# Kernel optimization log

Measured on AMD Instinct MI355X. Metric: run time of the kernel, lower is better.

## Reference

```python
import jax, jax.numpy as jnp
import numpy as np

B, T1, S, M = 64, 129, 128, 32   # batch, time-major dim, seq_len, num_series
U = 256                           # SkipGRUUnits
SKIP = 4                          # skip
HW = 128                          # highway window (== S by shape constraints)


def _skip_lstm(x_seq, kernel, rkernel, kernel2, bias, bias2, s0, units, skip):
    """Run the bespoke skip-LSTM cell over time. x_seq: (B, T, D) -> (B, T, U)."""
    Bx = x_seq.shape[0]
    # precompute input projections for all timesteps: (B, T, 4U)
    xW = jnp.einsum('btd,du->btu', x_seq, kernel) + bias
    # recurrent kernel viewed per-gate: Rk[:, g, :] == rkernel[:, g*U:(g+1)*U]
    Rk = rkernel.reshape(units, 4, units)

    def step(carry, x_t):
        h_tm1, c_tm1, prev_h = carry            # (B,4U), (B,U), (B,U*skip)
        x_i, x_f, x_c, x_o = jnp.split(x_t, 4, axis=1)
        hg = h_tm1.reshape(Bx, 4, units)        # gate-specific previous state
        r = jnp.einsum('bgu,ugv->bgv', hg, Rk)  # (B,4,U)
        i = jax.nn.sigmoid(x_i + r[:, 0])
        f = jax.nn.sigmoid(x_f + r[:, 1])
        c = f * c_tm1 + i * jnp.tanh(x_c + r[:, 2])
        o = jax.nn.sigmoid(x_o + r[:, 3])
        h = o * jnp.tanh(c)
        h_skip = jax.nn.sigmoid(prev_h[:, :units] @ kernel2 + bias2)
        h = s0 * h + (1.0 - s0) * h_skip
        new_h_tm1 = jnp.concatenate([i, f, c, o], axis=1)
        new_prev = jnp.concatenate([prev_h[:, units:], h], axis=1)
        return (new_h_tm1, c, new_prev), h

    init = (jnp.zeros((Bx, 4 * units), x_seq.dtype),
            jnp.zeros((Bx, units), x_seq.dtype),
            jnp.zeros((Bx, units * skip), x_seq.dtype))
    _, hs = jax.lax.scan(step, init, jnp.swapaxes(xW, 0, 1))  # (T,B,U)
    return jnp.swapaxes(hs, 0, 1)


def setup_inputs() -> dict:
    key = jax.random.key(0)
    ks = jax.random.split(key, 10)
    g = lambda k, shape, s=0.05: (jax.random.normal(k, shape, jnp.float32) * s)
    return {
        'X': jax.random.normal(ks[0], (B, T1, S, M), jnp.float32),
        'enc_kernel': g(ks[1], (M, 4 * U)),
        'enc_rkernel': g(ks[2], (U, 4 * U)),
        'enc_kernel2': g(ks[3], (U, U)),
        'enc_bias': jnp.zeros((4 * U,), jnp.float32),
        'enc_bias2': jnp.zeros((U,), jnp.float32),
        'enc_s0': jnp.float32(0.5),
        'dec_kernel': g(ks[4], (U, 4 * U)),
        'dec_rkernel': g(ks[5], (U, 4 * U)),
        'dec_kernel2': g(ks[6], (U, U)),
        'dec_bias': jnp.zeros((4 * U,), jnp.float32),
        'dec_bias2': jnp.zeros((U,), jnp.float32),
        'dec_s0': jnp.float32(0.5),
        'dense_w': g(ks[7], (S * U, S * M), 0.01),
        'dense_b': jnp.zeros((S * M,), jnp.float32),
        'final_w': g(ks[8], (HW,), 0.05),
        'final_b': jnp.zeros((), jnp.float32),
    }


def reference(X, enc_kernel, enc_rkernel, enc_kernel2, enc_bias, enc_bias2, enc_s0,
              dec_kernel, dec_rkernel, dec_kernel2, dec_bias, dec_bias2, dec_s0,
              dense_w, dense_b, final_w, final_b):
    X1 = X[:, 0]        # (B, S, M) encoder input
    X2 = X[:, 1:]       # (B, T1-1, S, M) highway inputs
    SE = _skip_lstm(X1, enc_kernel, enc_rkernel, enc_kernel2, enc_bias, enc_bias2, enc_s0, U, SKIP)
    SD = _skip_lstm(SE, dec_kernel, dec_rkernel, dec_kernel2, dec_bias, dec_bias2, dec_s0, U, SKIP)
    RD = SD.reshape(X.shape[0], S * U)
    Y = (RD @ dense_w + dense_b).reshape(-1, S, M)  # (B, S, M)
    # highway: PreARTrans takes last HW steps, shared final Linear(S->1) over time axis
    Z2 = jnp.einsum('bism,s->bim', X2[:, :, -HW:, :], final_w) + final_b  # (B, T1-1, M)
    return Y + Z2
```

## Files before the change

### kernel.cpp

```cpp
#include <hip/hip_runtime.h>
#include <hip/hip_fp16.h>


__device__ __forceinline__ float sigmoidf_(float x) {
    return 1.0f / (1.0f + __expf(-x));
}
__device__ __forceinline__ float tanhf_(float x) {
    float xc = fminf(fmaxf(x, -15.f), 15.f);
    float e = __expf(2.f * xc);
    return (e - 1.f) / (e + 1.f);
}
__device__ __forceinline__ unsigned pkh(float lo, float hi) {
    __half2 h = __halves2half2(__float2half(lo), __float2half(hi));
    return *reinterpret_cast<unsigned*>(&h);
}
__device__ __forceinline__ float2 uph(unsigned u) {
    __half2 h = *reinterpret_cast<__half2*>(&u);
    return __half22float2(h);
}

__global__ __launch_bounds__(256) void packall(
    const float* __restrict__ e_rk, const float* __restrict__ d_rk,
    const float* __restrict__ d_k,  const float* __restrict__ e_k,
    const float* __restrict__ e_k2, const float* __restrict__ d_k2,
    float4* __restrict__ rk4e, float4* __restrict__ rk4d,
    float4* __restrict__ dk4,  float4* __restrict__ ek4,
    unsigned* __restrict__ kh2e, unsigned* __restrict__ kh2d,
    unsigned* __restrict__ flags)
{
    const int bx = blockIdx.x, v = threadIdx.x;
    if (bx < 800) {
        const float* src; float4* dst; int row;
        if (bx < 256)      { src = e_rk; dst = rk4e; row = bx; }
        else if (bx < 512) { src = d_rk; dst = rk4d; row = bx - 256; }
        else if (bx < 768) { src = d_k;  dst = dk4;  row = bx - 512; }
        else               { src = e_k;  dst = ek4;  row = bx - 768; }
        const float* s = src + (size_t)row * 1024;
        dst[row * 256 + v] = make_float4(s[v], s[256 + v], s[512 + v], s[768 + v]);
    } else if (bx < 928) {
        const int u2 = bx - 800;
        kh2e[u2 * 256 + v] = pkh(e_k2[(2 * u2) * 256 + v], e_k2[(2 * u2 + 1) * 256 + v]);
        kh2d[u2 * 256 + v] = pkh(d_k2[(2 * u2) * 256 + v], d_k2[(2 * u2 + 1) * 256 + v]);
    } else {
        flags[v] = 0u;
    }
}

__global__ __launch_bounds__(256) void xw_gemm_enc(
    const float*  __restrict__ X,
    const float4* __restrict__ ek4,
    const float*  __restrict__ bias,
    float4* __restrict__ xWp)
{
    const int v = threadIdx.x;
    const int r0 = blockIdx.x * 16;
    __shared__ float se[16][32];

    #pragma unroll
    for (int p = 0; p < 2; ++p) {
        int idx = p * 256 + v;
        int rr = idx >> 5, d = idx & 31;
        int R = r0 + rr, b = R >> 7, t = R & 127;
        se[rr][d] = X[((size_t)b * 129 * 128 + t) * 32 + d];
    }
    __syncthreads();

    float4 bv = make_float4(bias[v], bias[256 + v], bias[512 + v], bias[768 + v]);
    float4 acc[16];
    #pragma unroll
    for (int rr = 0; rr < 16; ++rr) acc[rr] = bv;

    #pragma unroll
    for (int u = 0; u < 32; ++u) {
        float4 w = ek4[u * 256 + v];
        #pragma unroll
        for (int rr = 0; rr < 16; ++rr) {
            float s = se[rr][u];
            acc[rr].x += s * w.x; acc[rr].y += s * w.y;
            acc[rr].z += s * w.z; acc[rr].w += s * w.w;
        }
    }
    #pragma unroll
    for (int rr = 0; rr < 16; ++rr)
        xWp[(size_t)(r0 + rr) * 256 + v] = acc[rr];
}

__global__ __launch_bounds__(512) void xw_gemm_dec(
    const float*  __restrict__ SE,
    const float4* __restrict__ dk4,
    const float*  __restrict__ bias,
    float4* __restrict__ xWp)
{
    const int tid = threadIdx.x;
    const int v = tid & 255;
    const int hh = tid >> 8;
    const int rbase = blockIdx.x * 32;
    __shared__ float se[32][256];

    for (int i = tid; i < 8192; i += 512) {
        int rr = i >> 8, c = i & 255;
        se[rr][c] = SE[(size_t)(rbase + rr) * 256 + c];
    }
    __syncthreads();

    float4 bv = make_float4(bias[v], bias[256 + v], bias[512 + v], bias[768 + v]);
    float4 acc[16];
    #pragma unroll
    for (int rr = 0; rr < 16; ++rr) acc[rr] = bv;

    #pragma unroll 8
    for (int u = 0; u < 256; ++u) {
        float4 w = dk4[u * 256 + v];
        #pragma unroll
        for (int rr = 0; rr < 16; ++rr) {
            float s = se[hh * 16 + rr][u];
            acc[rr].x += s * w.x; acc[rr].y += s * w.y;
            acc[rr].z += s * w.z; acc[rr].w += s * w.w;
        }
    }
    #pragma unroll
    for (int rr = 0; rr < 16; ++rr)
        xWp[(size_t)(rbase + hh * 16 + rr) * 256 + v] = acc[rr];
}

__global__ __launch_bounds__(1024, 4) void rec9(
    const float4*   __restrict__ xW,
    const float4*   __restrict__ rk4,
    const unsigned* __restrict__ kh2,
    const float*    __restrict__ bias2,
    const float*    __restrict__ s0p,
    float* __restrict__ out,
    float* __restrict__ EX,
    unsigned* __restrict__ flags,
    unsigned fbase)
{
    const int b     = blockIdx.x & 63;
    const int slice = blockIdx.x >> 6;
    const int voff  = slice * 64;
    const int tid   = threadIdx.x;
    const int us    = tid >> 6;
    const int vl    = tid & 63;
    const int v     = voff + vl;

    __shared__ float4 wres[128][64];
    __shared__ float4 pA[16][64];
    __shared__ float  pS[16][64];
    __shared__ float4 h4[256];
    __shared__ float  pq[4][256];

    for (int i = tid; i < 8192; i += 1024) {
        int r = i >> 6, vv = i & 63;
        int cc = r >> 3, j = r & 7;
        wres[r][vv] = rk4[(cc * 16 + j) * 256 + voff + vv];
    }
    float4 wreg[8];
    unsigned kreg[8];
    {
        const float4*   wp = rk4 + (us * 16 + 8) * 256 + v;
        const unsigned* kp = kh2 + (us * 8) * 256 + v;
        #pragma unroll
        for (int j = 0; j < 8; ++j) wreg[j] = wp[j * 256];
        #pragma unroll
        for (int j = 0; j < 8; ++j) kreg[j] = kp[j * 256];
    }
    if (tid < 256) {
        h4[tid] = make_float4(0.f, 0.f, 0.f, 0.f);
        pq[0][tid] = 0.f; pq[1][tid] = 0.f; pq[2][tid] = 0.f; pq[3][tid] = 0.f;
    }
    float cst = 0.f;
    const float s0 = s0p[0];
    const float b2 = bias2[voff + vl];
    unsigned* mflag = flags + b * 4 + slice;
    __syncthreads();

    for (int t = 0; t < 128; ++t) {
        float4 xa = make_float4(0.f, 0.f, 0.f, 0.f);
        if (tid < 64) xa = xW[((size_t)b * 128 + t) * 256 + voff + tid];
        if (t > 0 && tid < 3) {
            int ps = tid + (tid >= slice ? 1 : 0);
            const unsigned* pf = flags + b * 4 + ps;
            while (__hip_atomic_load(pf, __ATOMIC_RELAXED, __HIP_MEMORY_SCOPE_AGENT) < fbase + (unsigned)t)
                __builtin_amdgcn_s_sleep(2);
        }
        __syncthreads();
        if (t > 0) {
            const int sp = (t + 1) & 1;
            if (tid < 480) {
                int pi = tid / 160;
                int j  = tid - pi * 160;
                int ps = pi + (pi >= slice ? 1 : 0);
                const unsigned long long* src = (const unsigned long long*)
                    (EX + (((size_t)sp * 64 + b) * 4 + ps) * 320);
                unsigned long long d = __hip_atomic_load(src + j, __ATOMIC_RELAXED, __HIP_MEMORY_SCOPE_AGENT);
                if (j < 128) {
                    reinterpret_cast<unsigned long long*>(&h4[ps * 64])[j] = d;
                } else {
                    int k = j - 128;
                    union { unsigned long long u; float f[2]; } cv; cv.u = d;
                    pq[(t + 3) & 3][ps * 64 + 2 * k]     = cv.f[0];
                    pq[(t + 3) & 3][ps * 64 + 2 * k + 1] = cv.f[1];
                }
            }
        }
        __syncthreads();

        float ai = 0.f, af = 0.f, acg = 0.f, ao = 0.f, as = 0.f;
        const int slot = t & 3;
        #pragma unroll
        for (int j = 0; j < 8; ++j) {
            float4 w = wres[us * 8 + j][vl];
            float4 g = h4[us * 16 + j];
            ai += g.x * w.x; af += g.y * w.y; acg += g.z * w.z; ao += g.w * w.w;
        }
        #pragma unroll
        for (int j = 0; j < 8; ++j) {
            float4 w = wreg[j];
            float4 g = h4[us * 16 + 8 + j];
            ai += g.x * w.x; af += g.y * w.y; acg += g.z * w.z; ao += g.w * w.w;
        }
        #pragma unroll
        for (int j = 0; j < 8; ++j) {
            float2 kk = uph(kreg[j]);
            as += pq[slot][us * 16 + 2 * j] * kk.x + pq[slot][us * 16 + 2 * j + 1] * kk.y;
        }
        pA[us][vl] = make_float4(ai, af, acg, ao);
        pS[us][vl] = as;
        __syncthreads();

        if (tid < 64) {
            float4 A = pA[0][vl];
            float  S = pS[0][vl];
            #pragma unroll
            for (int cc = 1; cc < 16; ++cc) {
                float4 q = pA[cc][vl];
                A.x += q.x; A.y += q.y; A.z += q.z; A.w += q.w;
                S += pS[cc][vl];
            }
            float gi = sigmoidf_(xa.x + A.x);
            float gf = sigmoidf_(xa.y + A.y);
            float cb = tanhf_(xa.z + A.z);
            cst = gf * cst + gi * cb;
            float go = sigmoidf_(xa.w + A.w);
            float hh = go * tanhf_(cst);
            float hs = sigmoidf_(S + b2);
            float hf = s0 * hh + (1.f - s0) * hs;
            h4[voff + vl] = make_float4(gi, gf, cst, go);
            pq[slot][voff + vl] = hf;
            out[((size_t)b * 128 + t) * 256 + voff + vl] = hf;
            float* dst = EX + (((size_t)(t & 1) * 64 + b) * 4 + slice) * 320;
            union { float4 f4; unsigned long long u[2]; } gv;
            gv.f4 = make_float4(gi, gf, cst, go);
            __hip_atomic_store((unsigned long long*)dst + 2 * vl,     gv.u[0], __ATOMIC_RELAXED, __HIP_MEMORY_SCOPE_AGENT);
            __hip_atomic_store((unsigned long long*)dst + 2 * vl + 1, gv.u[1], __ATOMIC_RELAXED, __HIP_MEMORY_SCOPE_AGENT);
            __hip_atomic_store(dst + 256 + vl, hf, __ATOMIC_RELAXED, __HIP_MEMORY_SCOPE_AGENT);
        }
        __syncthreads();
        if (tid == 0)
            __hip_atomic_store(mflag, fbase + (unsigned)(t + 1), __ATOMIC_RELAXED, __HIP_MEMORY_SCOPE_AGENT);
    }
}

__global__ __launch_bounds__(512, 4) void dense3(
    const float* __restrict__ SD,
    const float* __restrict__ dw,
    float* __restrict__ P)
{
    const int bid = blockIdx.x;
    const int kc = bid >> 5;
    const int bb = (bid >> 3) & 3;
    const int ct = bid & 7;
    const int tid = threadIdx.x;
    const int wv  = tid >> 6;
    const int wvj = wv & 1;
    const int wv2 = wv >> 1;
    const int lane = tid & 63;
    const int j0 = ct * 512 + wvj * 256 + lane * 4;
    const int kbase = kc * 2048;

    __shared__ float sst[16][68];
    __shared__ float red[4][4][520];

    float4 acc[16];
    #pragma unroll
    for (int b = 0; b < 16; ++b) acc[b] = make_float4(0.f, 0.f, 0.f, 0.f);

    for (int k0 = 0; k0 < 2048; k0 += 64) {
        if (tid < 256) {
            int r = tid >> 4, c4 = (tid & 15) * 4;
            float4 s4 = *reinterpret_cast<const float4*>(
                SD + (size_t)(bb * 16 + r) * 32768 + kbase + k0 + c4);
            sst[r][c4] = s4.x; sst[r][c4 + 1] = s4.y; sst[r][c4 + 2] = s4.z; sst[r][c4 + 3] = s4.w;
        }
        __syncthreads();
        #pragma unroll 2
        for (int kk = 0; kk < 16; ++kk) {
            const int krel = kk * 4 + wv2;
            float4 w4 = *reinterpret_cast<const float4*>(
                dw + (size_t)(kbase + k0 + krel) * 4096 + j0);
            #pragma unroll
            for (int b = 0; b < 16; ++b) {
                float s = sst[b][krel];
                acc[b].x += s * w4.x; acc[b].y += s * w4.y;
                acc[b].z += s * w4.z; acc[b].w += s * w4.w;
            }
        }
        __syncthreads();
    }

    for (int bg = 0; bg < 4; ++bg) {
        __syncthreads();
        #pragma unroll
        for (int i = 0; i < 4; ++i) {
            float4 a = acc[bg * 4 + i];
            float* d = &red[wv2][i][wvj * 256 + lane * 4];
            d[0] = a.x; d[1] = a.y; d[2] = a.z; d[3] = a.w;
        }
        __syncthreads();
        {
            int bi = tid >> 7;
            int jj = (tid & 127) * 4;
            float4 s;
            s.x = red[0][bi][jj]     + red[1][bi][jj]     + red[2][bi][jj]     + red[3][bi][jj];
            s.y = red[0][bi][jj + 1] + red[1][bi][jj + 1] + red[2][bi][jj + 1] + red[3][bi][jj + 1];
            s.z = red[0][bi][jj + 2] + red[1][bi][jj + 2] + red[2][bi][jj + 2] + red[3][bi][jj + 2];
            s.w = red[0][bi][jj + 3] + red[1][bi][jj + 3] + red[2][bi][jj + 3] + red[3][bi][jj + 3];
            *reinterpret_cast<float4*>(
                P + ((size_t)(kc * 64 + bb * 16 + bg * 4 + bi) * 4096) + ct * 512 + jj) = s;
        }
    }
}

__global__ __launch_bounds__(256) void reduce_z2(
    const float* __restrict__ P,
    const float* __restrict__ db,
    const float* __restrict__ X,
    const float* __restrict__ fw,
    const float* __restrict__ fbp,
    float* __restrict__ out)
{
    const int o4 = blockIdx.x * 256 + threadIdx.x;
    const int b  = o4 >> 10;
    const int j4 = o4 & 1023;
    const int j0 = j4 * 4;
    const int i  = j0 >> 5;
    const int m  = j0 & 31;

    float4 acc = *reinterpret_cast<const float4*>(db + j0);
    #pragma unroll
    for (int kc = 0; kc < 16; ++kc) {
        float4 p = *reinterpret_cast<const float4*>(P + (size_t)(kc * 64 + b) * 4096 + j0);
        acc.x += p.x; acc.y += p.y; acc.z += p.z; acc.w += p.w;
    }

    const float* xp = X + ((size_t)(b * 129 + 1 + i) * 128) * 32 + m;
    #pragma unroll 8
    for (int s = 0; s < 128; ++s) {
        float4 xv = *reinterpret_cast<const float4*>(xp + (size_t)s * 32);
        float w = fw[s];
        acc.x += w * xv.x; acc.y += w * xv.y; acc.z += w * xv.z; acc.w += w * xv.w;
    }
    const float fb = fbp[0];
    acc.x += fb; acc.y += fb; acc.z += fb; acc.w += fb;
    *reinterpret_cast<float4*>(out + (size_t)o4 * 4) = acc;
}

extern "C" void kernel_launch(void* const* d_in, const int* in_sizes, int n_in,
                              void* d_out, int out_size, void* d_ws, size_t ws_size,
                              hipStream_t stream) {
    const float* X    = (const float*)d_in[0];
    const float* e_k  = (const float*)d_in[1];
    const float* e_rk = (const float*)d_in[2];
    const float* e_k2 = (const float*)d_in[3];
    const float* e_b  = (const float*)d_in[4];
    const float* e_b2 = (const float*)d_in[5];
    const float* e_s0 = (const float*)d_in[6];
    const float* d_k  = (const float*)d_in[7];
    const float* d_rk = (const float*)d_in[8];
    const float* d_k2 = (const float*)d_in[9];
    const float* d_b  = (const float*)d_in[10];
    const float* d_b2 = (const float*)d_in[11];
    const float* d_s0 = (const float*)d_in[12];
    const float* dw   = (const float*)d_in[13];
    const float* db   = (const float*)d_in[14];
    const float* fw   = (const float*)d_in[15];
    const float* fb   = (const float*)d_in[16];

    float* ws = (float*)d_ws;
    float4*   rk4e  = (float4*)(ws);
    float4*   rk4d  = (float4*)(ws + 262144);
    float4*   dk4   = (float4*)(ws + 524288);
    float4*   ek4   = (float4*)(ws + 786432);
    unsigned* kh2e  = (unsigned*)(ws + 819200);
    unsigned* kh2d  = (unsigned*)(ws + 851968);
    float*    EX    = ws + 884736;
    unsigned* flags = (unsigned*)(ws + 1212416);
    float*    xW    = ws + 1310720;
    float*    SE    = ws + 9699328;
    float*    SD    = ws + 11796480;

    float* P = xW;

    hipLaunchKernelGGL(packall, dim3(929), dim3(256), 0, stream,
                       e_rk, d_rk, d_k, e_k, e_k2, d_k2,
                       rk4e, rk4d, dk4, ek4, kh2e, kh2d, flags);
    hipLaunchKernelGGL(xw_gemm_enc, dim3(512), dim3(256), 0, stream,
                       X, ek4, e_b, (float4*)xW);
    hipLaunchKernelGGL(rec9, dim3(256), dim3(1024), 0, stream,
                       (const float4*)xW, rk4e, kh2e, e_b2, e_s0, SE, EX, flags, 0u);
    hipLaunchKernelGGL(xw_gemm_dec, dim3(256), dim3(512), 0, stream,
                       SE, dk4, d_b, (float4*)xW);
    hipLaunchKernelGGL(rec9, dim3(256), dim3(1024), 0, stream,
                       (const float4*)xW, rk4d, kh2d, d_b2, d_s0, SD, EX, flags, 128u);
    hipLaunchKernelGGL(dense3, dim3(512), dim3(512), 0, stream, SD, dw, P);
    hipLaunchKernelGGL(reduce_z2, dim3(256), dim3(256), 0, stream,
                       P, db, X, fw, fb, (float*)d_out);
}
```

Baseline: 1.191 ms.

## Run the final dense projection on fp16 MFMA with a narrower split-K

```diff
diff --git a/kernel.cpp b/kernel.cpp
--- a/kernel.cpp
+++ b/kernel.cpp
@@ -1,6 +1,9 @@
 #include <hip/hip_runtime.h>
 #include <hip/hip_fp16.h>
 
+
+typedef _Float16 h8 __attribute__((ext_vector_type(8)));
+typedef float f4v __attribute__((ext_vector_type(4)));
 
 __device__ __forceinline__ float sigmoidf_(float x) {
     return 1.0f / (1.0f + __expf(-x));
@@ -260,72 +263,64 @@
     }
 }
 
-__global__ __launch_bounds__(512, 4) void dense3(
-    const float* __restrict__ SD,
-    const float* __restrict__ dw,
+__global__ __launch_bounds__(256) void cvt_sd(const float* __restrict__ SD, _Float16* __restrict__ SDh)
+{
+    const int i = (blockIdx.x * 256 + threadIdx.x) * 8;
+    float4 a = *reinterpret_cast<const float4*>(SD + i);
+    float4 b = *reinterpret_cast<const float4*>(SD + i + 4);
+    h8 h;
+    h[0] = (_Float16)a.x; h[1] = (_Float16)a.y; h[2] = (_Float16)a.z; h[3] = (_Float16)a.w;
+    h[4] = (_Float16)b.x; h[5] = (_Float16)b.y; h[6] = (_Float16)b.z; h[7] = (_Float16)b.w;
+    *reinterpret_cast<h8*>(SDh + i) = h;
+}
+
+__global__ __launch_bounds__(256, 4) void mfma_dense(
+    const _Float16* __restrict__ SDh,
+    const float*    __restrict__ dw,
     float* __restrict__ P)
 {
-    const int bid = blockIdx.x;
-    const int kc = bid >> 5;
-    const int bb = (bid >> 3) & 3;
-    const int ct = bid & 7;
+    const int nb  = blockIdx.x & 63;
+    const int kc  = blockIdx.x >> 6;
+    const int n0  = nb * 64;
     const int tid = threadIdx.x;
-    const int wv  = tid >> 6;
-    const int wvj = wv & 1;
-    const int wv2 = wv >> 1;
-    const int lane = tid & 63;
-    const int j0 = ct * 512 + wvj * 256 + lane * 4;
-    const int kbase = kc * 2048;
-
-    __shared__ float sst[16][68];
-    __shared__ float red[4][4][520];
-
-    float4 acc[16];
-    #pragma unroll
-    for (int b = 0; b < 16; ++b) acc[b] = make_float4(0.f, 0.f, 0.f, 0.f);
-
-    for (int k0 = 0; k0 < 2048; k0 += 64) {
-        if (tid < 256) {
-            int r = tid >> 4, c4 = (tid & 15) * 4;
-            float4 s4 = *reinterpret_cast<const float4*>(
-                SD + (size_t)(bb * 16 + r) * 32768 + kbase + k0 + c4);
-            sst[r][c4] = s4.x; sst[r][c4 + 1] = s4.y; sst[r][c4 + 2] = s4.z; sst[r][c4 + 3] = s4.w;
-        }
-        __syncthreads();
-        #pragma unroll 2
-        for (int kk = 0; kk < 16; ++kk) {
-            const int krel = kk * 4 + wv2;
-            float4 w4 = *reinterpret_cast<const float4*>(
-                dw + (size_t)(kbase + k0 + krel) * 4096 + j0);
+    const int w   = tid >> 6;
+    const int l   = tid & 63;
+    const int ar  = l & 15;
+    const int ko8 = (l >> 4) * 8;
+
+    __shared__ unsigned Bt[64][36];
+
+    f4v acc[4] = {{0.f,0.f,0.f,0.f},{0.f,0.f,0.f,0.f},{0.f,0.f,0.f,0.f},{0.f,0.f,0.f,0.f}};
+
+    for (int kk = 0; kk < 128; ++kk) {
+        const int kg = kc * 8192 + kk * 64;
+        #pragma unroll
+        for (int i = 0; i < 8; ++i) {
+            int k2 = w * 8 + i;
+            float lo = dw[(size_t)(kg + 2 * k2)     * 4096 + n0 + l];
+            float hi = dw[(size_t)(kg + 2 * k2 + 1) * 4096 + n0 + l];
+            Bt[l][k2] = pkh(lo, hi);
+        }
+        __syncthreads();
+        #pragma unroll
+        for (int hs = 0; hs < 2; ++hs) {
+            const int kw = kg + hs * 32;
+            h8 bf = *reinterpret_cast<const h8*>(
+                      reinterpret_cast<const _Float16*>(&Bt[16 * w + ar][0]) + hs * 32 + ko8);
             #pragma unroll
-            for (int b = 0; b < 16; ++b) {
-                float s = sst[b][krel];
-                acc[b].x += s * w4.x; acc[b].y += s * w4.y;
-                acc[b].z += s * w4.z; acc[b].w += s * w4.w;
+            for (int mt = 0; mt < 4; ++mt) {
+                h8 af = *reinterpret_cast<const h8*>(
+                          SDh + (size_t)(mt * 16 + ar) * 32768 + kw + ko8);
+                acc[mt] = __builtin_amdgcn_mfma_f32_16x16x32_f16(af, bf, acc[mt], 0, 0, 0);
             }
         }
         __syncthreads();
     }
-
-    for (int bg = 0; bg < 4; ++bg) {
-        __syncthreads();
-        #pragma unroll
-        for (int i = 0; i < 4; ++i) {
-            float4 a = acc[bg * 4 + i];
-            float* d = &red[wv2][i][wvj * 256 + lane * 4];
-            d[0] = a.x; d[1] = a.y; d[2] = a.z; d[3] = a.w;
-        }
-        __syncthreads();
-        {
-            int bi = tid >> 7;
-            int jj = (tid & 127) * 4;
-            float4 s;
-            s.x = red[0][bi][jj]     + red[1][bi][jj]     + red[2][bi][jj]     + red[3][bi][jj];
-            s.y = red[0][bi][jj + 1] + red[1][bi][jj + 1] + red[2][bi][jj + 1] + red[3][bi][jj + 1];
-            s.z = red[0][bi][jj + 2] + red[1][bi][jj + 2] + red[2][bi][jj + 2] + red[3][bi][jj + 2];
-            s.w = red[0][bi][jj + 3] + red[1][bi][jj + 3] + red[2][bi][jj + 3] + red[3][bi][jj + 3];
-            *reinterpret_cast<float4*>(
-                P + ((size_t)(kc * 64 + bb * 16 + bg * 4 + bi) * 4096) + ct * 512 + jj) = s;
+    #pragma unroll
+    for (int mt = 0; mt < 4; ++mt) {
+        #pragma unroll
+        for (int r = 0; r < 4; ++r) {
+            P[(size_t)(kc * 64 + mt * 16 + (l >> 4) * 4 + r) * 4096 + n0 + 16 * w + ar] = acc[mt][r];
         }
     }
 }
@@ -347,7 +342,7 @@
 
     float4 acc = *reinterpret_cast<const float4*>(db + j0);
     #pragma unroll
-    for (int kc = 0; kc < 16; ++kc) {
+    for (int kc = 0; kc < 4; ++kc) {
         float4 p = *reinterpret_cast<const float4*>(P + (size_t)(kc * 64 + b) * 4096 + j0);
         acc.x += p.x; acc.y += p.y; acc.z += p.z; acc.w += p.w;
     }
@@ -398,7 +393,8 @@
     float*    SE    = ws + 9699328;
     float*    SD    = ws + 11796480;
 
-    float* P = xW;
+    float*     P   = xW;
+    _Float16*  SDh = (_Float16*)(ws + 5505024);
 
     hipLaunchKernelGGL(packall, dim3(929), dim3(256), 0, stream,
                        e_rk, d_rk, d_k, e_k, e_k2, d_k2,
@@ -411,7 +407,8 @@
                        SE, dk4, d_b, (float4*)xW);
     hipLaunchKernelGGL(rec9, dim3(256), dim3(1024), 0, stream,
                        (const float4*)xW, rk4d, kh2d, d_b2, d_s0, SD, EX, flags, 128u);
-    hipLaunchKernelGGL(dense3, dim3(512), dim3(512), 0, stream, SD, dw, P);
+    hipLaunchKernelGGL(cvt_sd, dim3(1024), dim3(256), 0, stream, SD, SDh);
+    hipLaunchKernelGGL(mfma_dense, dim3(256), dim3(256), 0, stream, SDh, dw, P);
     hipLaunchKernelGGL(reduce_z2, dim3(256), dim3(256), 0, stream,
                        P, db, X, fw, fb, (float*)d_out);
 }
```

New measurement: 1.163 ms. -2.4%, faster.
